# Performance work log

Hardware: AMD Instinct MI355X
Metric: run time of the kernel (lower is better)

## Reference

```python
import math
import jax, jax.numpy as jnp
import numpy as np


def _bilinear_maps_sample(kv_feats, shapes_wh, start_ids, locs, map_ids):
    """Bilinear sampling from concatenated multi-level 2D maps.

    kv_feats: [BH, S, C] flattened (row-major, per level) feature maps
    shapes_wh: [L, 2] int (W, H) per level
    start_ids: [L] int start offset of each level in S
    locs: [BH, M, 2] normalized (x, y) in [0, 1]
    map_ids: [BH, M] int level index per sample
    returns [BH, M, C]
    """
    wh = shapes_wh[map_ids]                      # [BH, M, 2]
    W = wh[..., 0]
    H = wh[..., 1]
    start = start_ids[map_ids]                   # [BH, M]
    Wf = W.astype(locs.dtype)
    Hf = H.astype(locs.dtype)
    x = locs[..., 0] * Wf - 0.5                  # align_corners=False convention
    y = locs[..., 1] * Hf - 0.5
    x0 = jnp.floor(x)
    y0 = jnp.floor(y)
    out = jnp.zeros(locs.shape[:-1] + (kv_feats.shape[-1],), kv_feats.dtype)
    for dx in (0, 1):
        for dy in (0, 1):
            xi = x0 + dx
            yi = y0 + dy
            w = (1.0 - jnp.abs(x - xi)) * (1.0 - jnp.abs(y - yi))
            valid = (xi >= 0) & (xi < Wf) & (yi >= 0) & (yi < Hf)
            xi_c = jnp.clip(xi, 0, Wf - 1).astype(jnp.int32)
            yi_c = jnp.clip(yi, 0, Hf - 1).astype(jnp.int32)
            idx = start + yi_c * W + xi_c        # [BH, M]
            f = jnp.take_along_axis(kv_feats, idx[..., None], axis=1)
            out = out + jnp.where(valid, w, 0.0)[..., None] * f
    return out


def setup_inputs() -> dict:
    key = jax.random.key(0)
    ks = jax.random.split(key, 10)
    B, N, L, Hh, P = 2, 2048, 5, 8, 4
    in_size, sample_size = 256, 256
    qk_size, value_size = 256, 256
    kv_size = qk_size + value_size

    shapes = np.array([[128, 128], [64, 64], [32, 32], [16, 16], [8, 8]], np.int32)  # (H, W)
    flat = (shapes[:, 0] * shapes[:, 1]).astype(np.int64)
    start = np.concatenate([[0], np.cumsum(flat)[:-1]]).astype(np.int32)
    S = int(flat.sum())  # 21824

    # sampling_offsets bias: canonical Deformable-DETR grid init
    thetas = np.arange(Hh, dtype=np.float32) * (2.0 * math.pi / Hh)
    grid = np.stack([np.cos(thetas), np.sin(thetas)], axis=1)
    grid = grid / np.abs(grid).max(axis=1, keepdims=True)
    grid = np.tile(grid.reshape(Hh, 1, 1, 2), (1, L, 1, 1))
    sizes = np.arange(1, P + 1, dtype=np.float32).reshape(1, 1, P, 1)
    b_off = (sizes * grid).reshape(-1)           # [H*L*P*2]

    def lin(k, out_d, in_d):
        return jax.random.normal(k, (out_d, in_d), jnp.float32) * (1.0 / math.sqrt(in_d))

    return {
        "in_feats": jax.random.normal(ks[0], (B, N, in_size), jnp.float32),
        "sample_priors": jax.random.uniform(ks[1], (B, N, L, 2), jnp.float32),
        "sample_feats": jax.random.normal(ks[2], (B, S, sample_size), jnp.float32),
        "sample_map_shapes": jnp.asarray(shapes),
        "sample_map_start_ids": jnp.asarray(start),
        "W_off": jax.random.normal(ks[3], (Hh * L * P * 2, in_size), jnp.float32) * 0.02,
        "b_off": jnp.asarray(b_off),
        "W_q": lin(ks[4], qk_size, in_size),
        "b_q": jnp.zeros((qk_size,), jnp.float32),
        "W_kv": lin(ks[5], kv_size, sample_size),
        "b_kv": jnp.zeros((kv_size,), jnp.float32),
        "point_encs": jax.random.normal(ks[6], (Hh, L * P, qk_size // Hh), jnp.float32) * 0.02,
        "W_out": lin(ks[7], in_size, value_size),
        "b_out": jnp.zeros((in_size,), jnp.float32),
    }


def reference(in_feats, sample_priors, sample_feats, sample_map_shapes,
              sample_map_start_ids, W_off, b_off, W_q, b_q, W_kv, b_kv,
              point_encs, W_out, b_out):
    B, N = in_feats.shape[:2]
    Hh, LP, dqk = point_encs.shape
    L = sample_map_shapes.shape[0]
    P = LP // L

    # sampling offsets + locations (priors last dim == 2 path)
    off = (in_feats @ W_off.T + b_off).reshape(B, N, Hh, L, P, 2)
    shapes_wh = sample_map_shapes[:, ::-1]                      # fliplr -> (W, H)
    norm = shapes_wh.astype(in_feats.dtype)[None, None, None, :, None, :]
    locs = sample_priors[:, :, None, :, None, :] + off / norm    # [B,N,H,L,P,2]

    q = (in_feats @ W_q.T + b_q).reshape(B, N, Hh, dqk)
    kv = sample_feats @ W_kv.T + b_kv                            # [B,S,kv_size]
    ck = kv.shape[-1] // Hh
    kv = kv.reshape(B, -1, Hh, ck).transpose(0, 2, 1, 3).reshape(B * Hh, -1, ck)

    locs = locs.transpose(0, 2, 1, 3, 4, 5).reshape(B * Hh, N * L * P, 2)
    map_ids = jnp.broadcast_to(jnp.arange(L, dtype=jnp.int32)[None, None, :, None],
                               (B * Hh, N, L, P)).reshape(B * Hh, -1)

    sampled = _bilinear_maps_sample(kv, shapes_wh, sample_map_start_ids, locs, map_ids)
    sampled = sampled.reshape(B, Hh, N, LP, ck).transpose(0, 2, 1, 3, 4)  # [B,N,H,LP,ck]

    keys = sampled[..., :dqk] + point_encs                       # [B,N,H,LP,dqk]
    vals = sampled[..., dqk:]                                    # [B,N,H,LP,cv]
    attn = jax.nn.softmax(
        jnp.einsum('bnhd,bnhpd->bnhp', q / math.sqrt(dqk), keys), axis=-1)
    weighted = jnp.einsum('bnhp,bnhpd->bnhd', attn, vals).reshape(B, N, -1)
    return weighted @ W_out.T + b_out
```

## Files before the change

kernel.cpp:

```cpp
#include <hip/hip_runtime.h>
#include <cstddef>

#define B_  2
#define N_  2048
#define L_  5
#define HH  8
#define P_  4
#define S_  21824
#define DQK 32

using bf16x8 = __attribute__((ext_vector_type(8))) short;
using f32x4  = __attribute__((ext_vector_type(4))) float;
using us8    = __attribute__((ext_vector_type(8))) unsigned short;

__device__ __forceinline__ unsigned short f2b(float f) {
  unsigned u = __builtin_bit_cast(unsigned, f);
  u += 0x7FFFu + ((u >> 16) & 1u);
  return (unsigned short)(u >> 16);
}
__device__ __forceinline__ float b2f(unsigned short h) {
  return __builtin_bit_cast(float, ((unsigned)h) << 16);
}
__device__ __forceinline__ unsigned cvtpk(float lo, float hi) {
  unsigned r;
  asm("v_cvt_pk_bf16_f32 %0, %1, %2" : "=v"(r) : "v"(lo), "v"(hi));
  return r;
}

__device__ __forceinline__ void gld_lds16(const void* g, void* l) {
  __builtin_amdgcn_global_load_lds(
      (const __attribute__((address_space(1))) unsigned int*)g,
      (__attribute__((address_space(3))) unsigned int*)l, 16, 0, 0);
}

template <int CTRL>
__device__ __forceinline__ float dppadd(float v) {
  const int x = __builtin_bit_cast(int, v);
  return v + __builtin_bit_cast(float,
      __builtin_amdgcn_update_dpp(x, x, CTRL, 0xF, 0xF, false));
}

#define E0 1396736
#define E1 1527808
#define E2 1658880
#define E3 1675264
#define E4 1683456
#define E5 1691648
#define E6 1703936
#define E7 1716224

__device__ __forceinline__ void cvt8_plain(const float* s, unsigned short* d, int u) {
  const float4 a = ((const float4*)s)[2 * u];
  const float4 b = ((const float4*)s)[2 * u + 1];
  us8 o;
  o[0] = f2b(a.x); o[1] = f2b(a.y); o[2] = f2b(a.z); o[3] = f2b(a.w);
  o[4] = f2b(b.x); o[5] = f2b(b.y); o[6] = f2b(b.z); o[7] = f2b(b.w);
  ((us8*)d)[u] = o;
}
__device__ __forceinline__ unsigned short f2b_lo(float x) {
  return f2b(x - b2f(f2b(x)));
}
__device__ __forceinline__ void cvt8_lo(const float* s, unsigned short* d, int u) {
  const float4 a = ((const float4*)s)[2 * u];
  const float4 b = ((const float4*)s)[2 * u + 1];
  us8 o;
  o[0] = f2b_lo(a.x); o[1] = f2b_lo(a.y); o[2] = f2b_lo(a.z); o[3] = f2b_lo(a.w);
  o[4] = f2b_lo(b.x); o[5] = f2b_lo(b.y); o[6] = f2b_lo(b.z); o[7] = f2b_lo(b.w);
  ((us8*)d)[u] = o;
}

__global__ __launch_bounds__(256) void cvt_all(
    const float* __restrict__ sfeats, const float* __restrict__ in_feats,
    const float* __restrict__ W_kv, const float* __restrict__ W_q,
    const float* __restrict__ W_out, const float* __restrict__ W_off,
    unsigned short* __restrict__ sf_bf, unsigned short* __restrict__ if_hi,
    unsigned short* __restrict__ if_lo, unsigned short* __restrict__ wkv_bf,
    unsigned short* __restrict__ wq_bf, unsigned short* __restrict__ wout_bf,
    unsigned short* __restrict__ woff_hi, unsigned short* __restrict__ woff_lo) {
  const int i = blockIdx.x * 256 + threadIdx.x;
  if      (i < E0) cvt8_plain(sfeats, sf_bf, i);
  else if (i < E1) cvt8_plain(in_feats, if_hi, i - E0);
  else if (i < E2) cvt8_lo(in_feats, if_lo, i - E1);
  else if (i < E3) cvt8_plain(W_kv, wkv_bf, i - E2);
  else if (i < E4) cvt8_plain(W_q, wq_bf, i - E3);
  else if (i < E5) cvt8_plain(W_out, wout_bf, i - E4);
  else if (i < E6) {
    const int u = i - E5;
    if ((u >> 5) < 320) cvt8_plain(W_off, woff_hi, u);
    else ((us8*)woff_hi)[u] = (us8)0;
  } else {
    const int u = i - E6;
    if ((u >> 5) < 320) cvt8_lo(W_off, woff_lo, u);
    else ((us8*)woff_lo)[u] = (us8)0;
  }
}

__device__ __forceinline__ void mfma_compute(
    const unsigned short* As, const unsigned short* Bs,
    int wr, int wc, int fr, int fq, f32x4 (&acc)[4][4]) {
#pragma unroll
  for (int kk = 0; kk < 2; ++kk) {
    bf16x8 af[4], bfv[4];
#pragma unroll
    for (int i = 0; i < 4; ++i) {
      const int ar = wr * 64 + i * 16 + fr;
      const int cha = (kk * 4 + fq) ^ (ar & 7);
      af[i] = *(const bf16x8*)(As + ar * 64 + cha * 8);
      const int br = wc * 64 + i * 16 + fr;
      const int chb = (kk * 4 + fq) ^ (br & 7);
      bfv[i] = *(const bf16x8*)(Bs + br * 64 + chb * 8);
    }
#pragma unroll
    for (int i = 0; i < 4; ++i)
#pragma unroll
      for (int j = 0; j < 4; ++j)
        acc[i][j] = __builtin_amdgcn_mfma_f32_16x16x32_bf16(
            af[i], bfv[j], acc[i][j], 0, 0, 0);
  }
}

__device__ __forceinline__ void mfma_tile_bf16(
    const unsigned short* __restrict__ Ap, const unsigned short* __restrict__ Wp,
    unsigned short* As, unsigned short* Bs,
    int row0, int col0, int wv, int wr, int wc, int fr, int fq,
    int srow, int sch, f32x4 (&acc)[4][4]) {
  for (int k0 = 0; k0 < 256; k0 += 64) {
#pragma unroll
    for (int i = 0; i < 4; ++i) {
      const int r = i * 32 + srow;
      const int ca = sch ^ (r & 7);
      gld_lds16(Ap + (size_t)(row0 + r) * 256 + k0 + ca * 8,
                As + (size_t)(i * 32 + wv * 8) * 64);
      gld_lds16(Wp + (size_t)(col0 + r) * 256 + k0 + ca * 8,
                Bs + (size_t)(i * 32 + wv * 8) * 64);
    }
    __syncthreads();
    mfma_compute(As, Bs, wr, wc, fr, fq, acc);
    __syncthreads();
  }
}

__global__ __launch_bounds__(256) void ubergemm(
    const unsigned short* __restrict__ sf_bf,
    const unsigned short* __restrict__ wkv_bf,
    const unsigned short* __restrict__ if_hi,
    const unsigned short* __restrict__ if_lo,
    const unsigned short* __restrict__ woff_hi,
    const unsigned short* __restrict__ woff_lo,
    const unsigned short* __restrict__ wq_bf,
    const float* __restrict__ b_kv, const float* __restrict__ b_off,
    const float* __restrict__ b_q,
    unsigned short* __restrict__ kvt, float* __restrict__ offb,
    float* __restrict__ qb) {
  __shared__ __align__(16) unsigned short lds[128 * 128];

  const int tid = threadIdx.x;
  const int lane = tid & 63;
  const int wv = tid >> 6;
  const int wr = wv >> 1, wc = wv & 1;
  const int fr = lane & 15, fq = lane >> 4;
  const int bx = blockIdx.x;

  f32x4 acc[4][4] = {};

  if (bx >= 160) {
    const int t = bx - 160;
    const int x = t & 7;
    const int idx = t >> 3;
    const int c = idx & 3;
    const int g = (idx >> 2) * 8 + x;
    if (g >= 341) return;
    const int row0 = g * 128;
    const int col0 = c * 128;

    unsigned short* Ab[2] = {lds, lds + 4096};
    unsigned short* Bb[2] = {lds + 8192, lds + 12288};

#define KV_STAGE(KK, BUF)                                                     \
    {                                                                         \
      _Pragma("unroll")                                                       \
      for (int ld = 0; ld < 2; ++ld) {                                        \
        const int ci = ld * 256 + tid;                                        \
        const int rw = ci >> 2, cc = ci & 3;                                  \
        const int ca = cc ^ (rw & 3);                                         \
        gld_lds16(sf_bf + (size_t)(row0 + rw) * 256 + (KK) * 32 + ca * 8,     \
                  Ab[BUF] + (size_t)(ld * 256 + wv * 64) * 8);                \
        gld_lds16(wkv_bf + (size_t)(col0 + rw) * 256 + (KK) * 32 + ca * 8,    \
                  Bb[BUF] + (size_t)(ld * 256 + wv * 64) * 8);                \
      }                                                                       \
    }

    KV_STAGE(0, 0);
#pragma unroll
    for (int k = 0; k < 8; ++k) {
      if (k < 7) {
        KV_STAGE(k + 1, (k + 1) & 1);
        asm volatile("s_waitcnt vmcnt(4)" ::: "memory");
      } else {
        asm volatile("s_waitcnt vmcnt(0)" ::: "memory");
      }
      __builtin_amdgcn_s_barrier();
      __builtin_amdgcn_sched_barrier(0);
      const unsigned short* Ac = Ab[k & 1];
      const unsigned short* Bc = Bb[k & 1];
      bf16x8 af[4], bfv[4];
#pragma unroll
      for (int i = 0; i < 4; ++i) {
        const int ar = wr * 64 + i * 16 + fr;
        af[i] = *(const bf16x8*)(Ac + (ar * 4 + (fq ^ (ar & 3))) * 8);
      }
#pragma unroll
      for (int j = 0; j < 4; ++j) {
        const int nr = wc * 64 + j * 16 + fr;
        bfv[j] = *(const bf16x8*)(Bc + (nr * 4 + (fq ^ (nr & 3))) * 8);
      }
#pragma unroll
      for (int j = 0; j < 4; ++j)
#pragma unroll
        for (int i = 0; i < 4; ++i)
          acc[j][i] = __builtin_amdgcn_mfma_f32_16x16x32_bf16(
              bfv[j], af[i], acc[j][i], 0, 0, 0);
      __builtin_amdgcn_s_barrier();
    }
#undef KV_STAGE

#pragma unroll
    for (int j = 0; j < 4; ++j) {
      const int c0 = col0 + wc * 64 + j * 16 + fq * 4;
      const float4 bb = *(const float4*)(b_kv + c0);
      const int h = c0 >> 6;
      const int cc = c0 & 63;
#pragma unroll
      for (int i = 0; i < 4; ++i) {
        const int sl = row0 + wr * 64 + i * 16 + fr;
        const int b = (sl >= S_) ? 1 : 0;
        const int s = sl - b * S_;
        unsigned* dst = (unsigned*)(kvt + ((size_t)(b * HH + h) * S_ + s) * 64 + cc);
        dst[0] = cvtpk(acc[j][i][0] + bb.x, acc[j][i][1] + bb.y);
        dst[1] = cvtpk(acc[j][i][2] + bb.z, acc[j][i][3] + bb.w);
      }
    }
    return;
  }

  unsigned short* As = lds;
  unsigned short* Bs = lds + 128 * 64;
  const int srow = tid >> 3;
  const int sch = tid & 7;
  int row0, col0, ldc, nbias;
  const float* bias;
  float* Cf;
  if (bx < 96) {
    col0 = (bx % 3) * 128; row0 = (bx / 3) * 128;
    bias = b_off; Cf = offb; ldc = 384; nbias = 320;
    mfma_tile_bf16(if_hi, woff_hi, As, Bs, row0, col0, wv, wr, wc, fr, fq, srow, sch, acc);
    mfma_tile_bf16(if_hi, woff_lo, As, Bs, row0, col0, wv, wr, wc, fr, fq, srow, sch, acc);
    mfma_tile_bf16(if_lo, woff_hi, As, Bs, row0, col0, wv, wr, wc, fr, fq, srow, sch, acc);
  } else {
    const int t = bx - 96;
    col0 = (t & 1) * 128; row0 = (t >> 1) * 128;
    bias = b_q; Cf = qb; ldc = 256; nbias = 256;
    mfma_tile_bf16(if_hi, wq_bf, As, Bs, row0, col0, wv, wr, wc, fr, fq, srow, sch, acc);
  }

#pragma unroll
  for (int j = 0; j < 4; ++j) {
    const int n = col0 + wc * 64 + j * 16 + fr;
    const float bv = (n < nbias) ? bias[n] : 0.f;
#pragma unroll
    for (int i = 0; i < 4; ++i) {
      const int mbase = row0 + wr * 64 + i * 16 + fq * 4;
#pragma unroll
      for (int r = 0; r < 4; ++r)
        Cf[(size_t)(mbase + r) * ldc + n] = acc[i][j][r] + bv;
    }
  }
}

__global__ __launch_bounds__(256) void gemm_out(
    const unsigned short* __restrict__ A, const unsigned short* __restrict__ Wt,
    const float* __restrict__ bias, float* __restrict__ C) {
  __shared__ __align__(16) unsigned short As[128 * 64];
  __shared__ __align__(16) unsigned short Bs[128 * 64];
  const int tid = threadIdx.x;
  const int lane = tid & 63;
  const int wv = tid >> 6;
  const int wr = wv >> 1, wc = wv & 1;
  const int fr = lane & 15, fq = lane >> 4;
  const int row0 = blockIdx.y * 128, col0 = blockIdx.x * 128;
  const int srow = tid >> 3, sch = tid & 7;
  f32x4 acc[4][4] = {};
  mfma_tile_bf16(A, Wt, As, Bs, row0, col0, wv, wr, wc, fr, fq, srow, sch, acc);
#pragma unroll
  for (int j = 0; j < 4; ++j) {
    const int n = col0 + wc * 64 + j * 16 + fr;
    const float bv = bias[n];
#pragma unroll
    for (int i = 0; i < 4; ++i) {
      const int mbase = row0 + wr * 64 + i * 16 + fq * 4;
#pragma unroll
      for (int r = 0; r < 4; ++r)
        C[(size_t)(mbase + r) * 256 + n] = acc[i][j][r] + bv;
    }
  }
}

__global__ __launch_bounds__(256) void sample_attn4(
    const unsigned short* __restrict__ kvt,
    const float* __restrict__ offb,
    const float* __restrict__ qb,
    const float* __restrict__ priors,
    const int* __restrict__ shapes,
    const int* __restrict__ starts,
    const float* __restrict__ pencs,
    unsigned short* __restrict__ wtd) {
  __shared__ __align__(16) int pbuf[4][20][8];
  const int wv = threadIdx.x >> 6;
  const int lane = threadIdx.x & 63;
  const int beta = blockIdx.x;
  const int sig = (beta & 7) * 2 + ((beta >> 3) & 1);
  const int chunk = beta >> 4;
  const int h = sig & 7;
  const int b = sig >> 3;
  const int bn = b * N_ + chunk * 4 + wv;
  const int j = lane & 31;
  const int half = lane >> 5;

  if (lane < 20) {
    const int pp = lane;
    const int l = pp >> 2;
    const float2 oxy = *(const float2*)(offb + (size_t)bn * 384 + h * 40 + pp * 2);
    const float2 pxy = *(const float2*)(priors + ((size_t)bn * 5 + l) * 2);
    const int Wd = shapes[l * 2 + 1];
    const int Hd = shapes[l * 2 + 0];
    const int st = starts[l];
    const float Wf = (float)Wd, Hf = (float)Hd;
    const float x = (pxy.x + oxy.x / Wf) * Wf - 0.5f;
    const float y = (pxy.y + oxy.y / Hf) * Hf - 0.5f;
    const float x0f = floorf(x), y0f = floorf(y);
    const float fx = x - x0f, fy = y - y0f;
    const int xi = (int)x0f, yi = (int)y0f;
    int a[4]; float w[4];
#pragma unroll
    for (int dy = 0; dy < 2; ++dy)
#pragma unroll
      for (int dx = 0; dx < 2; ++dx) {
        const int xc = xi + dx, yc = yi + dy;
        const bool valid = (xc >= 0) & (xc < Wd) & (yc >= 0) & (yc < Hd);
        const float wt = (dx ? fx : 1.f - fx) * (dy ? fy : 1.f - fy);
        const int xcc = min(max(xc, 0), Wd - 1);
        const int ycc = min(max(yc, 0), Hd - 1);
        a[dy * 2 + dx] = (st + ycc * Wd + xcc) * 32;
        w[dy * 2 + dx] = valid ? wt : 0.f;
      }
    *(int4*)&pbuf[wv][pp][0] = make_int4(a[0], a[1], a[2], a[3]);
    *(float4*)&pbuf[wv][pp][4] = make_float4(w[0], w[1], w[2], w[3]);
  }

  const int jc = j & 15;
  float2 q2 = *(const float2*)(qb + (size_t)bn * 256 + h * DQK + 2 * jc);
  q2.x *= 0.17677669529663687f;
  q2.y *= 0.17677669529663687f;
  float qpe[10];
#pragma unroll
  for (int i = 0; i < 10; ++i) {
    const float2 pe = *(const float2*)(
        pencs + ((size_t)h * 20 + 2 * i + half) * DQK + 2 * jc);
    qpe[i] = q2.x * pe.x + q2.y * pe.y;
  }

  const unsigned* kvd = (const unsigned*)(kvt + (size_t)(b * HH + h) * (S_ * 64));
  int4 aa[2]; float4 ww[2]; unsigned g[2][4];
  aa[0] = *(const int4*)&pbuf[wv][half][0];
  ww[0] = *(const float4*)&pbuf[wv][half][4];
  g[0][0] = kvd[(unsigned)aa[0].x + j];
  g[0][1] = kvd[(unsigned)aa[0].y + j];
  g[0][2] = kvd[(unsigned)aa[0].z + j];
  g[0][3] = kvd[(unsigned)aa[0].w + j];

  float2 sam[10];
  float lg[10];
#pragma unroll
  for (int i = 0; i < 10; ++i) {
    const int cur = i & 1, nxt = cur ^ 1;
    if (i < 9) {
      aa[nxt] = *(const int4*)&pbuf[wv][2 * (i + 1) + half][0];
      ww[nxt] = *(const float4*)&pbuf[wv][2 * (i + 1) + half][4];
      g[nxt][0] = kvd[(unsigned)aa[nxt].x + j];
      g[nxt][1] = kvd[(unsigned)aa[nxt].y + j];
      g[nxt][2] = kvd[(unsigned)aa[nxt].z + j];
      g[nxt][3] = kvd[(unsigned)aa[nxt].w + j];
    }
    const float4 wt = ww[cur];
    const unsigned g0 = g[cur][0], g1 = g[cur][1], g2 = g[cur][2], g3 = g[cur][3];
    const float lo0 = __builtin_bit_cast(float, g0 << 16);
    const float hi0 = __builtin_bit_cast(float, g0 & 0xFFFF0000u);
    const float lo1 = __builtin_bit_cast(float, g1 << 16);
    const float hi1 = __builtin_bit_cast(float, g1 & 0xFFFF0000u);
    const float lo2 = __builtin_bit_cast(float, g2 << 16);
    const float hi2 = __builtin_bit_cast(float, g2 & 0xFFFF0000u);
    const float lo3 = __builtin_bit_cast(float, g3 << 16);
    const float hi3 = __builtin_bit_cast(float, g3 & 0xFFFF0000u);
    float vx = wt.x * lo0;  vx = fmaf(wt.y, lo1, vx);
    vx = fmaf(wt.z, lo2, vx); vx = fmaf(wt.w, lo3, vx);
    float vy = wt.x * hi0;  vy = fmaf(wt.y, hi1, vy);
    vy = fmaf(wt.z, hi2, vy); vy = fmaf(wt.w, hi3, vy);
    sam[i].x = vx; sam[i].y = vy;
    float part = (j < 16) ? fmaf(q2.x, vx, fmaf(q2.y, vy, qpe[i])) : 0.f;
    part = dppadd<0xB1>(part);
    part = dppadd<0x4E>(part);
    part = dppadd<0x124>(part);
    part = dppadd<0x128>(part);
    lg[i] = part + __shfl_xor(part, 16, 64);
  }

  float mx = lg[0];
#pragma unroll
  for (int i = 1; i < 10; ++i) mx = fmaxf(mx, lg[i]);
  mx = fmaxf(mx, __shfl_xor(mx, 32, 64));
  float se = 0.f;
#pragma unroll
  for (int i = 0; i < 10; ++i) {
    lg[i] = __expf(lg[i] - mx);
    se += lg[i];
  }
  se += __shfl_xor(se, 32, 64);
  const float inv = 1.f / se;

  float ax = 0.f, ay = 0.f;
#pragma unroll
  for (int i = 0; i < 10; ++i) {
    ax = fmaf(lg[i], sam[i].x, ax);
    ay = fmaf(lg[i], sam[i].y, ay);
  }
  ax += __shfl_xor(ax, 32, 64);
  ay += __shfl_xor(ay, 32, 64);

  if (half == 0 && j >= 16) {
    const unsigned u = (unsigned)f2b(ax * inv) | ((unsigned)f2b(ay * inv) << 16);
    ((unsigned*)wtd)[(size_t)bn * 128 + h * 16 + (j - 16)] = u;
  }
}

extern "C" void kernel_launch(void* const* d_in, const int* in_sizes, int n_in,
                              void* d_out, int out_size, void* d_ws, size_t ws_size,
                              hipStream_t stream) {
  const float* in_feats = (const float*)d_in[0];
  const float* priors   = (const float*)d_in[1];
  const float* sfeats   = (const float*)d_in[2];
  const int*   shapes   = (const int*)d_in[3];
  const int*   starts   = (const int*)d_in[4];
  const float* W_off    = (const float*)d_in[5];
  const float* b_off    = (const float*)d_in[6];
  const float* W_q      = (const float*)d_in[7];
  const float* b_q      = (const float*)d_in[8];
  const float* W_kv     = (const float*)d_in[9];
  const float* b_kv     = (const float*)d_in[10];
  const float* pencs    = (const float*)d_in[11];
  const float* W_out    = (const float*)d_in[12];
  const float* b_out    = (const float*)d_in[13];
  float* out = (float*)d_out;

  char* w = (char*)d_ws;
  unsigned short* kvt = (unsigned short*)w;
  w += (size_t)B_ * HH * S_ * 64 * 2;
  unsigned short* sf_bf = (unsigned short*)w;
  w += (size_t)B_ * S_ * 256 * 2;
  unsigned short* if_hi = (unsigned short*)w; w += (size_t)4096 * 256 * 2;
  unsigned short* if_lo = (unsigned short*)w; w += (size_t)4096 * 256 * 2;
  unsigned short* wkv_bf = (unsigned short*)w;  w += (size_t)512 * 256 * 2;
  unsigned short* wq_bf  = (unsigned short*)w;  w += (size_t)256 * 256 * 2;
  unsigned short* wout_bf = (unsigned short*)w; w += (size_t)256 * 256 * 2;
  unsigned short* woff_hi = (unsigned short*)w; w += (size_t)384 * 256 * 2;
  unsigned short* woff_lo = (unsigned short*)w; w += (size_t)384 * 256 * 2;
  float* offb = (float*)w;  w += (size_t)4096 * 384 * 4;
  float* qb   = (float*)w;  w += (size_t)4096 * 256 * 4;
  unsigned short* wtd_bf = (unsigned short*)w; w += (size_t)4096 * 256 * 2;

  cvt_all<<<E7 / 256, 256, 0, stream>>>(
      sfeats, in_feats, W_kv, W_q, W_out, W_off,
      sf_bf, if_hi, if_lo, wkv_bf, wq_bf, wout_bf, woff_hi, woff_lo);

  ubergemm<<<1536, 256, 0, stream>>>(
      sf_bf, wkv_bf, if_hi, if_lo, woff_hi, woff_lo, wq_bf,
      b_kv, b_off, b_q, kvt, offb, qb);

  sample_attn4<<<(B_ * N_ * HH) / 4, 256, 0, stream>>>(
      kvt, offb, qb, priors, shapes, starts, pencs, wtd_bf);

  gemm_out<<<dim3(2, 32), 256, 0, stream>>>(wtd_bf, wout_bf, b_out, out);
}
```

Baseline: 87.09 us.

## Deepen gather prefetch to five stages and remap block-to-head order

The sampling kernel now issues the gathers for the first five sample pairs up front and refills each slot with the pair five steps ahead, where it previously used a two-deep ping-pong. More loads are in flight to hide gather latency, at the cost of more registers. The block index mapping also changes so consecutive blocks walk over token chunks within each (batch, head) pair rather than interleaving the batch halves. This is meant to alter L2 locality of the kv table.

```diff
diff --git a/kernel.cpp b/kernel.cpp
--- a/kernel.cpp
+++ b/kernel.cpp
@@ -305,7 +305,7 @@
   }
 }
 
-__global__ __launch_bounds__(256) void sample_attn4(
+__global__ __launch_bounds__(256) void sample_attn5(
     const unsigned short* __restrict__ kvt,
     const float* __restrict__ offb,
     const float* __restrict__ qb,
@@ -318,8 +318,8 @@
   const int wv = threadIdx.x >> 6;
   const int lane = threadIdx.x & 63;
   const int beta = blockIdx.x;
-  const int sig = (beta & 7) * 2 + ((beta >> 3) & 1);
-  const int chunk = beta >> 4;
+  const int sig = (beta & 7) * 2 + (beta >> 12);
+  const int chunk = (beta >> 3) & 511;
   const int h = sig & 7;
   const int b = sig >> 3;
   const int bn = b * N_ + chunk * 4 + wv;
@@ -370,29 +370,34 @@
   }
 
   const unsigned* kvd = (const unsigned*)(kvt + (size_t)(b * HH + h) * (S_ * 64));
-  int4 aa[2]; float4 ww[2]; unsigned g[2][4];
-  aa[0] = *(const int4*)&pbuf[wv][half][0];
-  ww[0] = *(const float4*)&pbuf[wv][half][4];
-  g[0][0] = kvd[(unsigned)aa[0].x + j];
-  g[0][1] = kvd[(unsigned)aa[0].y + j];
-  g[0][2] = kvd[(unsigned)aa[0].z + j];
-  g[0][3] = kvd[(unsigned)aa[0].w + j];
+
+  float4 wwp[5];
+  unsigned g[5][4];
+#pragma unroll
+  for (int i = 0; i < 5; ++i) {
+    const int4 aa = *(const int4*)&pbuf[wv][2 * i + half][0];
+    wwp[i] = *(const float4*)&pbuf[wv][2 * i + half][4];
+    g[i][0] = kvd[(unsigned)aa.x + j];
+    g[i][1] = kvd[(unsigned)aa.y + j];
+    g[i][2] = kvd[(unsigned)aa.z + j];
+    g[i][3] = kvd[(unsigned)aa.w + j];
+  }
 
   float2 sam[10];
   float lg[10];
 #pragma unroll
   for (int i = 0; i < 10; ++i) {
-    const int cur = i & 1, nxt = cur ^ 1;
-    if (i < 9) {
-      aa[nxt] = *(const int4*)&pbuf[wv][2 * (i + 1) + half][0];
-      ww[nxt] = *(const float4*)&pbuf[wv][2 * (i + 1) + half][4];
-      g[nxt][0] = kvd[(unsigned)aa[nxt].x + j];
-      g[nxt][1] = kvd[(unsigned)aa[nxt].y + j];
-      g[nxt][2] = kvd[(unsigned)aa[nxt].z + j];
-      g[nxt][3] = kvd[(unsigned)aa[nxt].w + j];
-    }
-    const float4 wt = ww[cur];
-    const unsigned g0 = g[cur][0], g1 = g[cur][1], g2 = g[cur][2], g3 = g[cur][3];
+    const int s = i % 5;
+    const float4 wt = wwp[s];
+    const unsigned g0 = g[s][0], g1 = g[s][1], g2 = g[s][2], g3 = g[s][3];
+    if (i < 5) {
+      const int4 aa = *(const int4*)&pbuf[wv][2 * (i + 5) + half][0];
+      wwp[s] = *(const float4*)&pbuf[wv][2 * (i + 5) + half][4];
+      g[s][0] = kvd[(unsigned)aa.x + j];
+      g[s][1] = kvd[(unsigned)aa.y + j];
+      g[s][2] = kvd[(unsigned)aa.z + j];
+      g[s][3] = kvd[(unsigned)aa.w + j];
+    }
     const float lo0 = __builtin_bit_cast(float, g0 << 16);
     const float hi0 = __builtin_bit_cast(float, g0 & 0xFFFF0000u);
     const float lo1 = __builtin_bit_cast(float, g1 << 16);
@@ -485,7 +490,7 @@
       sf_bf, wkv_bf, if_hi, if_lo, woff_hi, woff_lo, wq_bf,
       b_kv, b_off, b_q, kvt, offb, qb);
 
-  sample_attn4<<<(B_ * N_ * HH) / 4, 256, 0, stream>>>(
+  sample_attn5<<<(B_ * N_ * HH) / 4, 256, 0, stream>>>(
       kvt, offb, qb, priors, shapes, starts, pencs, wtd_bf);
 
   gemm_out<<<dim3(2, 32), 256, 0, stream>>>(wtd_bf, wout_bf, b_out, out);
```

After: 86.95 us. Within noise of the previous version (-0.2%).
